# Kernel tuning notes

Hardware: AMD Instinct MI355X
Metric: run time of the kernel (lower is better)

The kernel has to match this reference:

```python
import jax, jax.numpy as jnp
import numpy as np

MAX_WAVELENGTH = 10000
BIG_NEG = -2.3819763e38

def _rope(x, positions):
    # x: [B, L, H, D], positions: [B, L] float32
    d = x.shape[-1]
    freq_exp = 2.0 / d * jnp.arange(d // 2, dtype=jnp.float32)
    timescale = MAX_WAVELENGTH ** freq_exp
    radians = (positions[..., None] / timescale[None, None, :])[..., None, :]  # [B,L,1,D/2]
    sin, cos = jnp.sin(radians), jnp.cos(radians)
    x1, x2 = jnp.split(x, 2, axis=-1)
    return jnp.concatenate([x1 * cos - x2 * sin, x2 * cos + x1 * sin], axis=-1).astype(x.dtype)

def _adaln_rmsnorm(x, cond, Wmod, bmod):
    # RMSNorm in fp32, then AdaLN scale/shift; returns (normed, gate[B,1,D])
    var = jnp.mean(jnp.square(x.astype(jnp.float32)), axis=-1, keepdims=True)
    normed = x * jax.lax.rsqrt(var + 1e-6)
    mod = (cond @ Wmod + bmod)[:, None, :]  # [B,1,3D]
    scale, shift, gate = jnp.split(mod, 3, axis=-1)
    return (normed * (1 + scale) + shift).astype(x.dtype), gate

def setup_inputs() -> dict:
    key = jax.random.key(0)
    ks = jax.random.split(key, 9)
    B, T, D, F, N, K, H = 2, 2048, 2048, 16384, 8, 1, 256
    x = jax.random.normal(ks[0], (B, T, D), jnp.float32)
    positions = jnp.broadcast_to(jnp.arange(T, dtype=jnp.float32), (B, T))
    attn_mask = jnp.broadcast_to(jnp.tril(jnp.ones((T, T), dtype=bool))[None, None], (B, 1, T, T))
    cond = jax.random.normal(ks[1], (B, D), jnp.float32)
    Wmod_a = jax.random.normal(ks[2], (D, 3 * D), jnp.float32) * 0.02
    bmod_a = jnp.zeros((3 * D,), jnp.float32)
    Wq = jax.random.normal(ks[3], (N, D, H), jnp.float32) * (D ** -0.5)
    Wkv = jax.random.normal(ks[4], (2, K, D, H), jnp.float32) * (D ** -0.5)
    Wo = jax.random.normal(ks[5], (N, H, D), jnp.float32) * ((N * H) ** -0.5)
    Wmod_f = jax.random.normal(ks[6], (D, 3 * D), jnp.float32) * 0.02
    bmod_f = jnp.zeros((3 * D,), jnp.float32)
    Wg = jax.random.normal(ks[7], (2, D, F), jnp.float32) * (D ** -0.5)
    Wl = jax.random.normal(ks[8], (F, D), jnp.float32) * (F ** -0.5)
    return dict(x=x, positions=positions, attn_mask=attn_mask, cond=cond,
                Wmod_a=Wmod_a, bmod_a=bmod_a, Wq=Wq, Wkv=Wkv, Wo=Wo,
                Wmod_f=Wmod_f, bmod_f=bmod_f, Wg=Wg, Wl=Wl)

def reference(x, positions, attn_mask, cond, Wmod_a, bmod_a, Wq, Wkv, Wo, Wmod_f, bmod_f, Wg, Wl):
    K = Wkv.shape[1]               # num_kv_heads
    H = Wq.shape[-1]               # head_dim
    # --- pre-attention AdaLN RMSNorm ---
    n, gate_a = _adaln_rmsnorm(x, cond, Wmod_a, bmod_a)
    # --- GQA projections ---
    q = jnp.einsum('BTD,NDH->BTNH', n, Wq)
    k = jnp.einsum('BSD,KDH->BSKH', n, Wkv[0])
    v = jnp.einsum('BSD,KDH->BSKH', n, Wkv[1])
    q = _rope(q, positions) * (H ** -0.5)
    k = _rope(k, positions)
    B, T, N, _ = q.shape
    q = q.reshape(B, T, K, N // K, H)  # B T K G H
    logits = jnp.einsum('BTKGH,BSKH->BKGTS', q, k, preferred_element_type=jnp.float32)
    masked = jnp.where(attn_mask[:, :, None, :, :], logits, BIG_NEG)
    probs = jax.nn.softmax(masked, axis=-1).astype(x.dtype)
    enc = jnp.einsum('BKGTS,BSKH->BTKGH', probs, v).reshape(B, T, N, H)
    attn_out = jnp.einsum('BTNH,NHD->BTD', enc, Wo)
    # gated residual
    x = x + attn_out * gate_a
    # --- pre-FFN AdaLN RMSNorm + gated-GeLU MLP ---
    n, gate_f = _adaln_rmsnorm(x, cond, Wmod_f, bmod_f)
    h = jax.nn.gelu(jnp.einsum('BTD,DF->BTF', n, Wg[0])) * jnp.einsum('BTD,DF->BTF', n, Wg[1])
    mlp_out = jnp.einsum('BTF,FD->BTD', h, Wl)
    return x + mlp_out * gate_f
```

## Files before the change

kernel.cpp:

```cpp
#include <hip/hip_runtime.h>
#include <hip/hip_bf16.h>

typedef __bf16 bf16_t;
typedef __bf16 bf16x8 __attribute__((ext_vector_type(8)));
typedef float  f32x4  __attribute__((ext_vector_type(4)));

#define DEV static __device__ __forceinline__

DEV void gload16(const bf16_t* g, bf16_t* l) {
    __builtin_amdgcn_global_load_lds(
        (const __attribute__((address_space(1))) void*)g,
        (__attribute__((address_space(3))) void*)l, 16, 0, 0);
}

enum { EPI_F32 = 0, EPI_BF16 = 1, EPI_RES = 2, EPI_GELU = 3, EPI_MUL = 4 };

template<int EPI>
__global__ __launch_bounds__(512, 1)
void gemm256(const bf16_t* __restrict__ A, const bf16_t* __restrict__ Bt,
             void* __restrict__ Cout, int Kd, int lda, int ldb, int ldc,
             long sCz,
             const float* __restrict__ res, const float* __restrict__ gate,
             int gateStride, int rowsPerB, const bf16_t* __restrict__ aux)
{
    const int nbx = gridDim.x;
    const int nwg = nbx * gridDim.y;
    int lin = blockIdx.y * nbx + blockIdx.x;
    const int q8 = nwg >> 3, r8 = nwg & 7;
    const int xcd = lin & 7, oo = lin >> 3;
    lin = (xcd < r8 ? xcd * (q8 + 1) : r8 * (q8 + 1) + (xcd - r8) * q8) + oo;
    const long m0 = (long)(lin / nbx) * 256;
    const long n0 = (long)(lin % nbx) * 256;
    const long kbase = (long)blockIdx.z * Kd;

    const int tid = threadIdx.x;
    const int l   = tid & 63;
    const int w   = tid >> 6;
    const int wr  = w >> 2;
    const int wcn = w & 3;

    __shared__ bf16_t sA[2][256 * 64];
    __shared__ bf16_t sB[2][256 * 64];

    const int  srow = w * 8 + (l >> 3);
    const long sgc  = (long)(((l & 7) ^ (l >> 3)) << 3);

    const int NT = Kd >> 6;

    auto STAGE = [&](const bf16_t* __restrict__ G, long row0, int ld, long kt, bf16_t* lb) {
#pragma unroll
        for (int L = 0; L < 4; L++) {
            const long g = (row0 + L * 64 + srow) * (long)ld + kt + sgc;
            gload16(G + g, lb + L * 4096 + w * 512);
        }
    };

    f32x4 acc[8][4];
#pragma unroll
    for (int i = 0; i < 8; i++)
#pragma unroll
        for (int j = 0; j < 4; j++) acc[i][j] = f32x4{0.f, 0.f, 0.f, 0.f};

    STAGE(A,  m0, lda, kbase, &sA[0][0]);
    STAGE(Bt, n0, ldb, kbase, &sB[0][0]);
    __syncthreads();

    const int co0 = ((l >> 4) ^ (l & 7)) << 3;
    const int co1 = ((4 + (l >> 4)) ^ (l & 7)) << 3;

    for (int t = 0; t < NT; ++t) {
        const int cur = t & 1;
        if (t + 1 < NT) {
            STAGE(A,  m0, lda, kbase + (long)(t + 1) * 64, &sA[cur ^ 1][0]);
            STAGE(Bt, n0, ldb, kbase + (long)(t + 1) * 64, &sB[cur ^ 1][0]);
        }
        const bf16_t* sAc = sA[cur];
        const bf16_t* sBc = sB[cur];
        bf16x8 a0[8], a1[8], b0[4], b1[4];
#pragma unroll
        for (int mi = 0; mi < 8; mi++) {
            const int row = wr * 128 + mi * 16 + (l & 15);
            a0[mi] = *(const bf16x8*)(&sAc[row * 64 + co0]);
            a1[mi] = *(const bf16x8*)(&sAc[row * 64 + co1]);
        }
#pragma unroll
        for (int nj = 0; nj < 4; nj++) {
            const int row = wcn * 64 + nj * 16 + (l & 15);
            b0[nj] = *(const bf16x8*)(&sBc[row * 64 + co0]);
            b1[nj] = *(const bf16x8*)(&sBc[row * 64 + co1]);
        }
#pragma unroll
        for (int mi = 0; mi < 8; mi++)
#pragma unroll
            for (int nj = 0; nj < 4; nj++)
                acc[mi][nj] = __builtin_amdgcn_mfma_f32_16x16x32_bf16(a0[mi], b0[nj], acc[mi][nj], 0, 0, 0);
#pragma unroll
        for (int mi = 0; mi < 8; mi++)
#pragma unroll
            for (int nj = 0; nj < 4; nj++)
                acc[mi][nj] = __builtin_amdgcn_mfma_f32_16x16x32_bf16(a1[mi], b1[nj], acc[mi][nj], 0, 0, 0);
        __syncthreads();
    }

#pragma unroll
    for (int mi = 0; mi < 8; mi++) {
#pragma unroll
        for (int nj = 0; nj < 4; nj++) {
            f32x4 v = acc[mi][nj];
            const long col   = n0 + wcn * 64 + nj * 16 + (l & 15);
            const long row0r = m0 + wr * 128 + mi * 16 + ((l >> 4) * 4);
#pragma unroll
            for (int e = 0; e < 4; e++) {
                const long row = row0r + e;
                const long idx = row * (long)ldc + col + (long)blockIdx.z * sCz;
                const float val = v[e];
                if constexpr (EPI == EPI_F32) {
                    ((float*)Cout)[idx] = val;
                } else if constexpr (EPI == EPI_BF16) {
                    ((bf16_t*)Cout)[idx] = (bf16_t)val;
                } else if constexpr (EPI == EPI_RES) {
                    const int b = (int)(row / rowsPerB);
                    ((float*)Cout)[idx] = res[row * (long)ldc + col] + val * gate[(long)b * gateStride + col];
                } else if constexpr (EPI == EPI_GELU) {
                    const float gl = 0.5f * val * (1.f + tanhf(0.7978845608f * (val + 0.044715f * val * val * val)));
                    ((bf16_t*)Cout)[idx] = (bf16_t)gl;
                } else if constexpr (EPI == EPI_MUL) {
                    ((bf16_t*)Cout)[idx] = (bf16_t)((float)aux[idx] * val);
                }
            }
        }
    }
}

__global__ __launch_bounds__(256)
void combine_splitk(const float* __restrict__ P, const float* __restrict__ X1,
                    const float* __restrict__ gate, float* __restrict__ out,
                    int D, int T, int gateStride, long zstride, long n4)
{
    for (long i4 = (long)blockIdx.x * 256 + threadIdx.x; i4 < n4; i4 += (long)gridDim.x * 256) {
        const long i = i4 * 4;
        const float4 p0 = *(const float4*)(P + i);
        const float4 p1 = *(const float4*)(P + i + zstride);
        const float4 xv = *(const float4*)(X1 + i);
        const long row = i / D;
        const int  b   = (int)(row / T);
        const int  col = (int)(i - row * D);
        const float* gp = gate + (long)b * gateStride + col;
        float4 r;
        r.x = xv.x + (p0.x + p1.x) * gp[0];
        r.y = xv.y + (p0.y + p1.y) * gp[1];
        r.z = xv.z + (p0.z + p1.z) * gp[2];
        r.w = xv.w + (p0.w + p1.w) * gp[3];
        *(float4*)(out + i) = r;
    }
}

template<int EPI, int CAUSAL>
__global__ __launch_bounds__(256)
void gemm_bt(const bf16_t* __restrict__ A, const bf16_t* __restrict__ Bt,
             void* __restrict__ Cout,
             int M, int N, int Kd, int lda, int ldb, int ldc,
             long sAz, long sBz, long sCz,
             const float* __restrict__ res, const float* __restrict__ gate,
             int gateStride, int rowsPerB, const bf16_t* __restrict__ aux)
{
    const int tid = threadIdx.x;
    const int l   = tid & 63;
    const int w   = tid >> 6;
    const int wr  = w >> 1, wc = w & 1;
    const long m0 = (long)blockIdx.y * 128;
    const long n0 = (long)blockIdx.x * 128;
    const int  z  = blockIdx.z;

    if constexpr (CAUSAL == 1) {
        if (n0 > m0 + 127) return;
    }
    int kend = Kd;
    if constexpr (CAUSAL == 2) {
        const int kc = (int)m0 + 128;
        kend = kc < Kd ? kc : Kd;
    }

    A  += (long)z * sAz;
    Bt += (long)z * sBz;

    __shared__ bf16_t As[128 * 32];
// ... 111 lines not shown
void rmsnorm_adaln(const float* __restrict__ xin, const float* __restrict__ mod,
                   bf16_t* __restrict__ out, int D, int T, int D3)
{
    const long row = blockIdx.x;
    const int  b   = (int)(row / T);
    const int  tid = threadIdx.x;
    const float4* x4 = (const float4*)(xin + row * (long)D);
    const float4 v0 = x4[tid], v1 = x4[tid + 256];
    float ss = v0.x * v0.x + v0.y * v0.y + v0.z * v0.z + v0.w * v0.w
             + v1.x * v1.x + v1.y * v1.y + v1.z * v1.z + v1.w * v1.w;
    for (int o = 32; o; o >>= 1) ss += __shfl_down(ss, o, 64);
    __shared__ float red[4];
    if ((tid & 63) == 0) red[tid >> 6] = ss;
    __syncthreads();
    ss = red[0] + red[1] + red[2] + red[3];
    const float rs = rsqrtf(ss / (float)D + 1e-6f);
    const float* sc = mod + (long)b * D3;
    const float* sh = sc + D;
    const float4 s0 = ((const float4*)sc)[tid], s1 = ((const float4*)sc)[tid + 256];
    const float4 h0 = ((const float4*)sh)[tid], h1 = ((const float4*)sh)[tid + 256];
    bf16_t* orow = out + row * (long)D;
    orow[tid * 4 + 0]         = (bf16_t)(v0.x * rs * (1.f + s0.x) + h0.x);
    orow[tid * 4 + 1]         = (bf16_t)(v0.y * rs * (1.f + s0.y) + h0.y);
    orow[tid * 4 + 2]         = (bf16_t)(v0.z * rs * (1.f + s0.z) + h0.z);
    orow[tid * 4 + 3]         = (bf16_t)(v0.w * rs * (1.f + s0.w) + h0.w);
    orow[(tid + 256) * 4 + 0] = (bf16_t)(v1.x * rs * (1.f + s1.x) + h1.x);
    orow[(tid + 256) * 4 + 1] = (bf16_t)(v1.y * rs * (1.f + s1.y) + h1.y);
    orow[(tid + 256) * 4 + 2] = (bf16_t)(v1.z * rs * (1.f + s1.z) + h1.z);
    orow[(tid + 256) * 4 + 3] = (bf16_t)(v1.w * rs * (1.f + s1.w) + h1.w);
}

__global__ __launch_bounds__(128)
void rope_q(const bf16_t* __restrict__ qp, const float* __restrict__ positions,
            bf16_t* __restrict__ qo, int T, int NH, int H)
{
    const int t = blockIdx.x, n = blockIdx.y, b = blockIdx.z;
    const int i = threadIdx.x;
    const long in0 = ((long)(b * T + t)) * NH + n * H;
    const float x1 = (float)qp[in0 + i];
    const float x2 = (float)qp[in0 + i + 128];
    const float pos = positions[b * T + t];
    const float inv = expf(-9.210340371976184f * (float)i / 128.f);
    float s, c;
    sincosf(pos * inv, &s, &c);
    const float scl = 0.0625f;
    const long out0 = (((long)(b * 8 + n)) * T + t) * H;
    qo[out0 + i]       = (bf16_t)((x1 * c - x2 * s) * scl);
    qo[out0 + i + 128] = (bf16_t)((x2 * c + x1 * s) * scl);
}

__global__ __launch_bounds__(128)
void rope_kv(const bf16_t* __restrict__ kvp, const float* __restrict__ positions,
             bf16_t* __restrict__ ko, bf16_t* __restrict__ vt, int T, int H, int S)
{
    const int t = blockIdx.x, b = blockIdx.y;
    const int i = threadIdx.x;
    const long in0 = ((long)(b * T + t)) * 512;
    const float k1 = (float)kvp[in0 + i];
    const float k2 = (float)kvp[in0 + i + 128];
    const float pos = positions[b * T + t];
    const float inv = expf(-9.210340371976184f * (float)i / 128.f);
    float s, c;
    sincosf(pos * inv, &s, &c);
    const long ko0 = ((long)(b * T + t)) * H;
    ko[ko0 + i]       = (bf16_t)(k1 * c - k2 * s);
    ko[ko0 + i + 128] = (bf16_t)(k2 * c + k1 * s);
    vt[((long)b * H + i) * S + t]       = kvp[in0 + 256 + i];
    vt[((long)b * H + i + 128) * S + t] = kvp[in0 + 256 + i + 128];
}

__global__ __launch_bounds__(256)
void softmax_causal(const float* __restrict__ sc, bf16_t* __restrict__ pr, int T, int S)
{
    const int t = blockIdx.x, g = blockIdx.y;
    const long row = (long)g * T + t;
    const float* srow = sc + row * S;
    bf16_t* prow = pr + row * S;
    const int tid = threadIdx.x;
    const int limit = t | 127;
    const int nch = (limit >> 8) + 1;
    float vals[8];
    float mx = -3.4e38f;
    for (int i = 0; i < nch; i++) {
        const int s = i * 256 + tid;
        const float v = (s <= t) ? srow[s] : -3.4e38f;
        vals[i] = v;
        mx = fmaxf(mx, v);
    }
    for (int o = 32; o; o >>= 1) mx = fmaxf(mx, __shfl_down(mx, o, 64));
    __shared__ float red[4];
// ... 7 lines not shown
        const float e = (s <= t) ? __expf(vals[i] - mx) : 0.f;
        vals[i] = e;
        sum += e;
    }
    for (int o = 32; o; o >>= 1) sum += __shfl_down(sum, o, 64);
    if ((tid & 63) == 0) red[tid >> 6] = sum;
    __syncthreads();
    sum = red[0] + red[1] + red[2] + red[3];
    const float invs = 1.f / sum;
    for (int i = 0; i < nch; i++)
        prow[i * 256 + tid] = (bf16_t)(vals[i] * invs);
}

extern "C" void kernel_launch(void* const* d_in, const int* in_sizes, int n_in,
                              void* d_out, int out_size, void* d_ws, size_t ws_size,
                              hipStream_t stream)
{
    const float* x      = (const float*)d_in[0];
    const float* pos    = (const float*)d_in[1];
    const float* cond   = (const float*)d_in[3];
    const float* Wmod_a = (const float*)d_in[4];
    const float* bmod_a = (const float*)d_in[5];
    const float* Wq     = (const float*)d_in[6];
    const float* Wkv    = (const float*)d_in[7];
    const float* Wo     = (const float*)d_in[8];
    const float* Wmod_f = (const float*)d_in[9];
    const float* bmod_f = (const float*)d_in[10];
    const float* Wg     = (const float*)d_in[11];
    const float* Wl     = (const float*)d_in[12];

    constexpr int  Bb = 2, T = 2048, D = 2048, F = 16384, Nh = 8, H = 256;
    constexpr int  NH = 2048, S = 2048, G = 8, BT = 4096, D3 = 6144;
    constexpr int  KSLICE = 64, NZ = D / KSLICE;

    char* ws = (char*)d_ws;
    size_t off = 0;
    auto alloc = [&](size_t bytes) { char* p = ws + off; off += bytes; return p; };

    bf16_t* WQT  = (bf16_t*)alloc((size_t)NH * D * 2);
    bf16_t* WKVT = (bf16_t*)alloc((size_t)512 * D * 2);
    bf16_t* WOT  = (bf16_t*)alloc((size_t)D * NH * 2);
    bf16_t* WGT  = (bf16_t*)alloc((size_t)2 * F * D * 2);
    bf16_t* WLT  = (bf16_t*)alloc((size_t)D * F * 2);
    float*  MODA = (float*)alloc((size_t)Bb * D3 * 4);
    float*  MODF = (float*)alloc((size_t)Bb * D3 * 4);
    float*  PART = (float*)alloc((size_t)NZ * Bb * D3 * 4);
    bf16_t* NA   = (bf16_t*)alloc((size_t)BT * D * 2);
    bf16_t* QP   = (bf16_t*)alloc((size_t)BT * NH * 2);
    bf16_t* KVP  = (bf16_t*)alloc((size_t)BT * 512 * 2);
    bf16_t* Qr   = (bf16_t*)alloc((size_t)Bb * Nh * T * H * 2);
    bf16_t* Kr   = (bf16_t*)alloc((size_t)Bb * T * H * 2);
    bf16_t* VT   = (bf16_t*)alloc((size_t)Bb * H * S * 2);
    bf16_t* ENC  = (bf16_t*)alloc((size_t)BT * NH * 2);
    float*  X1   = (float*)alloc((size_t)BT * D * 4);
    bf16_t* NF   = (bf16_t*)alloc((size_t)BT * D * 2);
    const size_t scBytes = (size_t)G * T * S * 4;
    const size_t prBytes = (size_t)G * T * S * 2;
    const size_t hBytes  = (size_t)BT * F * 2;
    const size_t bigBytes = (scBytes + prBytes > hBytes) ? (scBytes + prBytes) : hBytes;
    char* big = alloc(bigBytes);
    float*  SC = (float*)big;
    bf16_t* PR = (bf16_t*)(big + scBytes);
    bf16_t* Hb = (bf16_t*)big;
    float*  PARTK = (float*)(big + hBytes);
    (void)ws_size; (void)in_sizes; (void)n_in; (void)out_size;

    const dim3 tb(32, 8);
    transpose_f2b<<<dim3(H / 32, D / 32, 8), tb, 0, stream>>>(Wq,  WQT,  D,  H, (long)D * H, (long)H * D);
    transpose_f2b<<<dim3(H / 32, D / 32, 2), tb, 0, stream>>>(Wkv, WKVT, D,  H, (long)D * H, (long)H * D);
    transpose_f2b<<<dim3(D / 32, NH / 32, 1), tb, 0, stream>>>(Wo, WOT, NH,  D, 0, 0);
    transpose_f2b<<<dim3(F / 32, D / 32, 2), tb, 0, stream>>>(Wg,  WGT,  D,  F, (long)D * F, (long)F * D);
    transpose_f2b<<<dim3(D / 32, F / 32, 1), tb, 0, stream>>>(Wl,  WLT,  F,  D, 0, 0);
    modk_part<<<dim3(D3 / 256, Bb, NZ), 256, 0, stream>>>(cond, Wmod_a, PART, D3, KSLICE);
    modk_reduce<<<dim3(D3 / 256, Bb), 256, 0, stream>>>(PART, bmod_a, MODA, D3, NZ);
    modk_part<<<dim3(D3 / 256, Bb, NZ), 256, 0, stream>>>(cond, Wmod_f, PART, D3, KSLICE);
    modk_reduce<<<dim3(D3 / 256, Bb), 256, 0, stream>>>(PART, bmod_f, MODF, D3, NZ);
    rmsnorm_adaln<<<BT, 256, 0, stream>>>(x, MODA, NA, D, T, D3);
    gemm256<EPI_BF16><<<dim3(NH / 256, BT / 256, 1), 512, 0, stream>>>(
        NA, WQT, QP, D, D, D, NH, 0, nullptr, nullptr, 0, 0, nullptr);
    gemm_bt<EPI_BF16, 0><<<dim3(512 / 128, BT / 128, 1), 256, 0, stream>>>(
        NA, WKVT, KVP, BT, 512, D, D, D, 512, 0, 0, 0, nullptr, nullptr, 0, 0, nullptr);
    rope_q<<<dim3(T, Nh, Bb), 128, 0, stream>>>(QP, pos, Qr, T, NH, H);
    rope_kv<<<dim3(T, Bb), 128, 0, stream>>>(KVP, pos, Kr, VT, T, H, S);
    for (int b = 0; b < Bb; b++) {
        gemm_bt<EPI_F32, 1><<<dim3(S / 128, T / 128, G), 256, 0, stream>>>(
            Qr + (long)b * Nh * T * H, Kr + (long)b * T * H, SC,
            T, S, H, H, H, S, (long)T * H, 0, (long)T * S, nullptr, nullptr, 0, 0, nullptr);
        softmax_causal<<<dim3(T, G), 256, 0, stream>>>(SC, PR, T, S);
        gemm_bt<EPI_BF16, 2><<<dim3(H / 128, T / 128, G), 256, 0, stream>>>(
            PR, VT + (long)b * H * S, ENC + (long)b * T * NH,
            T, H, S, S, S, NH, (long)T * S, 0, (long)H, nullptr, nullptr, 0, 0, nullptr);
    }
    gemm256<EPI_RES><<<dim3(D / 256, BT / 256, 1), 512, 0, stream>>>(
        ENC, WOT, X1, NH, NH, NH, D, 0, x, MODA + 2 * D, D3, T, nullptr);
    rmsnorm_adaln<<<BT, 256, 0, stream>>>(X1, MODF, NF, D, T, D3);
    gemm256<EPI_GELU><<<dim3(F / 256, BT / 256, 1), 512, 0, stream>>>(
        NF, WGT, Hb, D, D, D, F, 0, nullptr, nullptr, 0, 0, nullptr);
    gemm256<EPI_MUL><<<dim3(F / 256, BT / 256, 1), 512, 0, stream>>>(
        NF, WGT + (long)F * D, Hb, D, D, D, F, 0, nullptr, nullptr, 0, 0, Hb);
    gemm256<EPI_F32><<<dim3(D / 256, BT / 256, 2), 512, 0, stream>>>(
        Hb, WLT, PARTK, F / 2, F, F, D, (long)BT * D, nullptr, nullptr, 0, 0, nullptr);
    combine_splitk<<<2048, 256, 0, stream>>>(
        PARTK, X1, MODF + 2 * D, (float*)d_out, D, T, D3, (long)BT * D, (long)BT * D / 4);
}
```

Measured before the change: 1.689 ms.

## Replace 256x256 GEMM with triple-buffered 256x128 tile kernel, drop split-K

Replaces the double-buffered 256x256 GEMM with a 256x128-tile kernel that uses three LDS buffers. It prefetches two K-tiles ahead, uses explicit vmcnt waits with raw barriers, and raises wave priority around the MFMA block. The final down-projection no longer uses split-K plus a combine kernel; it runs as a single-pass GEMM with a fused residual-gate epilogue. The smaller tiles give more workgroups and deeper prefetch, but they increase global traffic per FLOP, and the down-projection now has a long serial K loop.

```diff
diff --git a/kernel.cpp b/kernel.cpp
--- a/kernel.cpp
+++ b/kernel.cpp
@@ -17,9 +17,8 @@
 
 template<int EPI>
 __global__ __launch_bounds__(512, 1)
-void gemm256(const bf16_t* __restrict__ A, const bf16_t* __restrict__ Bt,
+void gemm_p3(const bf16_t* __restrict__ A, const bf16_t* __restrict__ Bt,
              void* __restrict__ Cout, int Kd, int lda, int ldb, int ldc,
-             long sCz,
              const float* __restrict__ res, const float* __restrict__ gate,
              int gateStride, int rowsPerB, const bf16_t* __restrict__ aux)
 {
@@ -30,56 +29,55 @@
     const int xcd = lin & 7, oo = lin >> 3;
     lin = (xcd < r8 ? xcd * (q8 + 1) : r8 * (q8 + 1) + (xcd - r8) * q8) + oo;
     const long m0 = (long)(lin / nbx) * 256;
-    const long n0 = (long)(lin % nbx) * 256;
-    const long kbase = (long)blockIdx.z * Kd;
+    const long n0 = (long)(lin % nbx) * 128;
 
     const int tid = threadIdx.x;
     const int l   = tid & 63;
     const int w   = tid >> 6;
-    const int wr  = w >> 2;
-    const int wcn = w & 3;
-
-    __shared__ bf16_t sA[2][256 * 64];
-    __shared__ bf16_t sB[2][256 * 64];
-
-    const int  srow = w * 8 + (l >> 3);
-    const long sgc  = (long)(((l & 7) ^ (l >> 3)) << 3);
-
+    const int wrm = w >> 1;
+    const int wcn = w & 1;
+
+    __shared__ bf16_t sA[3][16384];
+    __shared__ bf16_t sB[3][8192];
+
+    const long sgc = (long)(((l & 7) ^ (l >> 3)) << 3);
     const int NT = Kd >> 6;
 
-    auto STAGE = [&](const bf16_t* __restrict__ G, long row0, int ld, long kt, bf16_t* lb) {
-#pragma unroll
-        for (int L = 0; L < 4; L++) {
-            const long g = (row0 + L * 64 + srow) * (long)ld + kt + sgc;
-            gload16(G + g, lb + L * 4096 + w * 512);
-        }
+    auto STAGE = [&](long kt, int bi) {
+#pragma unroll
+        for (int L = 0; L < 4; L++)
+            gload16(A + (m0 + L * 64 + w * 8 + (l >> 3)) * (long)lda + kt + sgc,
+                    &sA[bi][L * 4096 + w * 512]);
+#pragma unroll
+        for (int L = 0; L < 2; L++)
+            gload16(Bt + (n0 + L * 64 + w * 8 + (l >> 3)) * (long)ldb + kt + sgc,
+                    &sB[bi][L * 4096 + w * 512]);
     };
 
-    f32x4 acc[8][4];
-#pragma unroll
-    for (int i = 0; i < 8; i++)
+    f32x4 acc[4][4];
+#pragma unroll
+    for (int i = 0; i < 4; i++)
 #pragma unroll
         for (int j = 0; j < 4; j++) acc[i][j] = f32x4{0.f, 0.f, 0.f, 0.f};
-
-    STAGE(A,  m0, lda, kbase, &sA[0][0]);
-    STAGE(Bt, n0, ldb, kbase, &sB[0][0]);
-    __syncthreads();
 
     const int co0 = ((l >> 4) ^ (l & 7)) << 3;
     const int co1 = ((4 + (l >> 4)) ^ (l & 7)) << 3;
 
+    STAGE(0, 0);
+    STAGE(64, 1);
+    asm volatile("s_waitcnt vmcnt(6)" ::: "memory");
+    __builtin_amdgcn_s_barrier();
+
     for (int t = 0; t < NT; ++t) {
-        const int cur = t & 1;
-        if (t + 1 < NT) {
-            STAGE(A,  m0, lda, kbase + (long)(t + 1) * 64, &sA[cur ^ 1][0]);
-            STAGE(Bt, n0, ldb, kbase + (long)(t + 1) * 64, &sB[cur ^ 1][0]);
-        }
-        const bf16_t* sAc = sA[cur];
-        const bf16_t* sBc = sB[cur];
-        bf16x8 a0[8], a1[8], b0[4], b1[4];
-#pragma unroll
-        for (int mi = 0; mi < 8; mi++) {
-            const int row = wr * 128 + mi * 16 + (l & 15);
+        const int bi = t % 3;
+        if (t + 2 < NT) STAGE((long)(t + 2) * 64, (t + 2) % 3);
+
+        const bf16_t* sAc = sA[bi];
+        const bf16_t* sBc = sB[bi];
+        bf16x8 a0[4], a1[4], b0[4], b1[4];
+#pragma unroll
+        for (int mi = 0; mi < 4; mi++) {
+            const int row = wrm * 64 + mi * 16 + (l & 15);
             a0[mi] = *(const bf16x8*)(&sAc[row * 64 + co0]);
             a1[mi] = *(const bf16x8*)(&sAc[row * 64 + co1]);
         }
@@ -89,30 +87,38 @@
             b0[nj] = *(const bf16x8*)(&sBc[row * 64 + co0]);
             b1[nj] = *(const bf16x8*)(&sBc[row * 64 + co1]);
         }
-#pragma unroll
-        for (int mi = 0; mi < 8; mi++)
+        __builtin_amdgcn_s_setprio(1);
+#pragma unroll
+        for (int mi = 0; mi < 4; mi++)
 #pragma unroll
             for (int nj = 0; nj < 4; nj++)
                 acc[mi][nj] = __builtin_amdgcn_mfma_f32_16x16x32_bf16(a0[mi], b0[nj], acc[mi][nj], 0, 0, 0);
 #pragma unroll
-        for (int mi = 0; mi < 8; mi++)
+        for (int mi = 0; mi < 4; mi++)
 #pragma unroll
             for (int nj = 0; nj < 4; nj++)
                 acc[mi][nj] = __builtin_amdgcn_mfma_f32_16x16x32_bf16(a1[mi], b1[nj], acc[mi][nj], 0, 0, 0);
-        __syncthreads();
-    }
-
-#pragma unroll
-    for (int mi = 0; mi < 8; mi++) {
+        __builtin_amdgcn_s_setprio(0);
+
+        if (t + 2 < NT) {
+            asm volatile("s_waitcnt vmcnt(6)" ::: "memory");
+        } else if (t + 1 < NT) {
+            asm volatile("s_waitcnt vmcnt(0)" ::: "memory");
+        }
+        __builtin_amdgcn_s_barrier();
+    }
+
+#pragma unroll
+    for (int mi = 0; mi < 4; mi++) {
 #pragma unroll
         for (int nj = 0; nj < 4; nj++) {
             f32x4 v = acc[mi][nj];
             const long col   = n0 + wcn * 64 + nj * 16 + (l & 15);
-            const long row0r = m0 + wr * 128 + mi * 16 + ((l >> 4) * 4);
+            const long row0r = m0 + wrm * 64 + mi * 16 + ((l >> 4) * 4);
 #pragma unroll
             for (int e = 0; e < 4; e++) {
                 const long row = row0r + e;
-                const long idx = row * (long)ldc + col + (long)blockIdx.z * sCz;
+                const long idx = row * (long)ldc + col;
                 const float val = v[e];
                 if constexpr (EPI == EPI_F32) {
                     ((float*)Cout)[idx] = val;
@@ -129,29 +135,6 @@
                 }
             }
         }
-    }
-}
-
-__global__ __launch_bounds__(256)
-void combine_splitk(const float* __restrict__ P, const float* __restrict__ X1,
-                    const float* __restrict__ gate, float* __restrict__ out,
-                    int D, int T, int gateStride, long zstride, long n4)
-{
-    for (long i4 = (long)blockIdx.x * 256 + threadIdx.x; i4 < n4; i4 += (long)gridDim.x * 256) {
-        const long i = i4 * 4;
-        const float4 p0 = *(const float4*)(P + i);
-        const float4 p1 = *(const float4*)(P + i + zstride);
-        const float4 xv = *(const float4*)(X1 + i);
-        const long row = i / D;
-        const int  b   = (int)(row / T);
-        const int  col = (int)(i - row * D);
-        const float* gp = gate + (long)b * gateStride + col;
-        float4 r;
-        r.x = xv.x + (p0.x + p1.x) * gp[0];
-        r.y = xv.y + (p0.y + p1.y) * gp[1];
-        r.z = xv.z + (p0.z + p1.z) * gp[2];
-        r.w = xv.w + (p0.w + p1.w) * gp[3];
-        *(float4*)(out + i) = r;
     }
 }
 
@@ -456,7 +439,6 @@
     float*  SC = (float*)big;
     bf16_t* PR = (bf16_t*)(big + scBytes);
     bf16_t* Hb = (bf16_t*)big;
-    float*  PARTK = (float*)(big + hBytes);
     (void)ws_size; (void)in_sizes; (void)n_in; (void)out_size;
 
     const dim3 tb(32, 8);
@@ -470,8 +452,8 @@
     modk_part<<<dim3(D3 / 256, Bb, NZ), 256, 0, stream>>>(cond, Wmod_f, PART, D3, KSLICE);
     modk_reduce<<<dim3(D3 / 256, Bb), 256, 0, stream>>>(PART, bmod_f, MODF, D3, NZ);
     rmsnorm_adaln<<<BT, 256, 0, stream>>>(x, MODA, NA, D, T, D3);
-    gemm256<EPI_BF16><<<dim3(NH / 256, BT / 256, 1), 512, 0, stream>>>(
-        NA, WQT, QP, D, D, D, NH, 0, nullptr, nullptr, 0, 0, nullptr);
+    gemm_p3<EPI_BF16><<<dim3(NH / 128, BT / 256), 512, 0, stream>>>(
+        NA, WQT, QP, D, D, D, NH, nullptr, nullptr, 0, 0, nullptr);
     gemm_bt<EPI_BF16, 0><<<dim3(512 / 128, BT / 128, 1), 256, 0, stream>>>(
         NA, WKVT, KVP, BT, 512, D, D, D, 512, 0, 0, 0, nullptr, nullptr, 0, 0, nullptr);
     rope_q<<<dim3(T, Nh, Bb), 128, 0, stream>>>(QP, pos, Qr, T, NH, H);
@@ -485,15 +467,13 @@
             PR, VT + (long)b * H * S, ENC + (long)b * T * NH,
             T, H, S, S, S, NH, (long)T * S, 0, (long)H, nullptr, nullptr, 0, 0, nullptr);
     }
-    gemm256<EPI_RES><<<dim3(D / 256, BT / 256, 1), 512, 0, stream>>>(
-        ENC, WOT, X1, NH, NH, NH, D, 0, x, MODA + 2 * D, D3, T, nullptr);
+    gemm_p3<EPI_RES><<<dim3(D / 128, BT / 256), 512, 0, stream>>>(
+        ENC, WOT, X1, NH, NH, NH, D, x, MODA + 2 * D, D3, T, nullptr);
     rmsnorm_adaln<<<BT, 256, 0, stream>>>(X1, MODF, NF, D, T, D3);
-    gemm256<EPI_GELU><<<dim3(F / 256, BT / 256, 1), 512, 0, stream>>>(
-        NF, WGT, Hb, D, D, D, F, 0, nullptr, nullptr, 0, 0, nullptr);
-    gemm256<EPI_MUL><<<dim3(F / 256, BT / 256, 1), 512, 0, stream>>>(
-        NF, WGT + (long)F * D, Hb, D, D, D, F, 0, nullptr, nullptr, 0, 0, Hb);
-    gemm256<EPI_F32><<<dim3(D / 256, BT / 256, 2), 512, 0, stream>>>(
-        Hb, WLT, PARTK, F / 2, F, F, D, (long)BT * D, nullptr, nullptr, 0, 0, nullptr);
-    combine_splitk<<<2048, 256, 0, stream>>>(
-        PARTK, X1, MODF + 2 * D, (float*)d_out, D, T, D3, (long)BT * D, (long)BT * D / 4);
-}
+    gemm_p3<EPI_GELU><<<dim3(F / 128, BT / 256), 512, 0, stream>>>(
+        NF, WGT, Hb, D, D, D, F, nullptr, nullptr, 0, 0, nullptr);
+    gemm_p3<EPI_MUL><<<dim3(F / 128, BT / 256), 512, 0, stream>>>(
+        NF, WGT + (long)F * D, Hb, D, D, D, F, nullptr, nullptr, 0, 0, Hb);
+    gemm_p3<EPI_RES><<<dim3(D / 128, BT / 256), 512, 0, stream>>>(
+        Hb, WLT, (float*)d_out, F, F, F, D, X1, MODF + 2 * D, D3, T, nullptr);
+}
```

Measured after the change: 1.956 ms. 15.8% more time.

## Rewrite 256x256 GEMM as 8-phase interleaved pipeline and fuse QKV projection

Applied to the files above, without the earlier changes.

Replaces the double-buffered GEMM main loop with an 8-phase schedule. Each phase loads a quarter of the A/B fragments from LDS, issues a few global->LDS chunk loads for upcoming K tiles, and runs 16 MFMAs under raised wave priority. Explicit vmcnt waits and barriers replace the per-tile __syncthreads. The goal is to overlap global loads, LDS reads and MFMA issue more finely. The Q and KV projections are also merged into one 2560-wide GEMM, which relies on the K/V weights sitting right after the Q weights in the workspace, and the rope kernels now take a row stride.

```diff
diff --git a/kernel.cpp b/kernel.cpp
--- a/kernel.cpp
+++ b/kernel.cpp
@@ -15,13 +15,43 @@
 
 enum { EPI_F32 = 0, EPI_BF16 = 1, EPI_RES = 2, EPI_GELU = 3, EPI_MUL = 4 };
 
+#define MFMA16(QQ, AR, BR)                                                    \
+  _Pragma("unroll")                                                           \
+  for (int nj = 0; nj < 4; nj++) {                                            \
+    acc[(QQ)*4+0][nj] = __builtin_amdgcn_mfma_f32_16x16x32_bf16(AR[0], BR[nj], acc[(QQ)*4+0][nj], 0, 0, 0); \
+    acc[(QQ)*4+1][nj] = __builtin_amdgcn_mfma_f32_16x16x32_bf16(AR[1], BR[nj], acc[(QQ)*4+1][nj], 0, 0, 0); \
+    acc[(QQ)*4+2][nj] = __builtin_amdgcn_mfma_f32_16x16x32_bf16(AR[2], BR[nj], acc[(QQ)*4+2][nj], 0, 0, 0); \
+    acc[(QQ)*4+3][nj] = __builtin_amdgcn_mfma_f32_16x16x32_bf16(AR[3], BR[nj], acc[(QQ)*4+3][nj], 0, 0, 0); \
+  }
+
+#define READA(SAc, QQ, CO, AR)                                                \
+  _Pragma("unroll")                                                           \
+  for (int mi = 0; mi < 4; mi++)                                              \
+    AR[mi] = *(const bf16x8*)(&SAc[(wr*128 + (QQ)*64 + mi*16 + (l & 15))*64 + (CO)]);
+
+#define READB(SBc, CO, BR)                                                    \
+  _Pragma("unroll")                                                           \
+  for (int nj = 0; nj < 4; nj++)                                              \
+    BR[nj] = *(const bf16x8*)(&SBc[(wcn*64 + nj*16 + (l & 15))*64 + (CO)]);
+
+#define PHASE(RD_STMT, QQ, AR, BR, STAGE_STMT, WAIT_STMT)                     \
+  { RD_STMT STAGE_STMT                                                        \
+    __builtin_amdgcn_s_barrier();                                             \
+    asm volatile("s_waitcnt lgkmcnt(0)" ::: "memory");                        \
+    __builtin_amdgcn_sched_barrier(0);                                        \
+    __builtin_amdgcn_s_setprio(1);                                            \
+    MFMA16(QQ, AR, BR);                                                       \
+    __builtin_amdgcn_s_setprio(0);                                            \
+    WAIT_STMT                                                                 \
+    __builtin_amdgcn_s_barrier(); }
+
 template<int EPI>
 __global__ __launch_bounds__(512, 1)
-void gemm256(const bf16_t* __restrict__ A, const bf16_t* __restrict__ Bt,
-             void* __restrict__ Cout, int Kd, int lda, int ldb, int ldc,
-             long sCz,
-             const float* __restrict__ res, const float* __restrict__ gate,
-             int gateStride, int rowsPerB, const bf16_t* __restrict__ aux)
+void gemm8p(const bf16_t* __restrict__ A, const bf16_t* __restrict__ Bt,
+            void* __restrict__ Cout, int Kd, int lda, int ldb, int ldc,
+            long sCz,
+            const float* __restrict__ res, const float* __restrict__ gate,
+            int gateStride, int rowsPerB, const bf16_t* __restrict__ aux)
 {
     const int nbx = gridDim.x;
     const int nwg = nbx * gridDim.y;
@@ -31,7 +61,7 @@
     lin = (xcd < r8 ? xcd * (q8 + 1) : r8 * (q8 + 1) + (xcd - r8) * q8) + oo;
     const long m0 = (long)(lin / nbx) * 256;
     const long n0 = (long)(lin % nbx) * 256;
-    const long kbase = (long)blockIdx.z * Kd;
+    const long kb = (long)blockIdx.z * Kd;
 
     const int tid = threadIdx.x;
     const int l   = tid & 63;
@@ -39,67 +69,67 @@
     const int wr  = w >> 2;
     const int wcn = w & 3;
 
-    __shared__ bf16_t sA[2][256 * 64];
-    __shared__ bf16_t sB[2][256 * 64];
-
-    const int  srow = w * 8 + (l >> 3);
-    const long sgc  = (long)(((l & 7) ^ (l >> 3)) << 3);
-
+    __shared__ bf16_t sA[2][16384];
+    __shared__ bf16_t sB[2][16384];
+
+    const long sgc = (long)(((l & 7) ^ (l >> 3)) << 3);
     const int NT = Kd >> 6;
-
-    auto STAGE = [&](const bf16_t* __restrict__ G, long row0, int ld, long kt, bf16_t* lb) {
-#pragma unroll
-        for (int L = 0; L < 4; L++) {
-            const long g = (row0 + L * 64 + srow) * (long)ld + kt + sgc;
-            gload16(G + g, lb + L * 4096 + w * 512);
-        }
+    const int NI = NT >> 1;
+
+    auto SCA = [&](long kt, int bi, int c) {
+        gload16(A + (m0 + c * 64 + w * 8 + (l >> 3)) * (long)lda + kt + sgc,
+                &sA[bi][c * 4096 + w * 512]);
     };
+    auto SCB = [&](long kt, int bi, int c) {
+        gload16(Bt + (n0 + c * 64 + w * 8 + (l >> 3)) * (long)ldb + kt + sgc,
+                &sB[bi][c * 4096 + w * 512]);
+    };
 
     f32x4 acc[8][4];
 #pragma unroll
     for (int i = 0; i < 8; i++)
 #pragma unroll
         for (int j = 0; j < 4; j++) acc[i][j] = f32x4{0.f, 0.f, 0.f, 0.f};
-
-    STAGE(A,  m0, lda, kbase, &sA[0][0]);
-    STAGE(Bt, n0, ldb, kbase, &sB[0][0]);
-    __syncthreads();
 
     const int co0 = ((l >> 4) ^ (l & 7)) << 3;
     const int co1 = ((4 + (l >> 4)) ^ (l & 7)) << 3;
 
-    for (int t = 0; t < NT; ++t) {
-        const int cur = t & 1;
-        if (t + 1 < NT) {
-            STAGE(A,  m0, lda, kbase + (long)(t + 1) * 64, &sA[cur ^ 1][0]);
-            STAGE(Bt, n0, ldb, kbase + (long)(t + 1) * 64, &sB[cur ^ 1][0]);
-        }
-        const bf16_t* sAc = sA[cur];
-        const bf16_t* sBc = sB[cur];
-        bf16x8 a0[8], a1[8], b0[4], b1[4];
-#pragma unroll
-        for (int mi = 0; mi < 8; mi++) {
-            const int row = wr * 128 + mi * 16 + (l & 15);
-            a0[mi] = *(const bf16x8*)(&sAc[row * 64 + co0]);
-            a1[mi] = *(const bf16x8*)(&sAc[row * 64 + co1]);
-        }
-#pragma unroll
-        for (int nj = 0; nj < 4; nj++) {
-            const int row = wcn * 64 + nj * 16 + (l & 15);
-            b0[nj] = *(const bf16x8*)(&sBc[row * 64 + co0]);
-            b1[nj] = *(const bf16x8*)(&sBc[row * 64 + co1]);
-        }
-#pragma unroll
-        for (int mi = 0; mi < 8; mi++)
-#pragma unroll
-            for (int nj = 0; nj < 4; nj++)
-                acc[mi][nj] = __builtin_amdgcn_mfma_f32_16x16x32_bf16(a0[mi], b0[nj], acc[mi][nj], 0, 0, 0);
-#pragma unroll
-        for (int mi = 0; mi < 8; mi++)
-#pragma unroll
-            for (int nj = 0; nj < 4; nj++)
-                acc[mi][nj] = __builtin_amdgcn_mfma_f32_16x16x32_bf16(a1[mi], b1[nj], acc[mi][nj], 0, 0, 0);
-        __syncthreads();
+    SCA(kb, 0, 0); SCA(kb, 0, 1); SCA(kb, 0, 2); SCA(kb, 0, 3);
+    SCB(kb, 0, 0); SCB(kb, 0, 1); SCB(kb, 0, 2); SCB(kb, 0, 3);
+    SCA(kb + 64, 1, 0); SCA(kb + 64, 1, 2); SCB(kb + 64, 1, 0); SCB(kb + 64, 1, 1);
+    asm volatile("s_waitcnt vmcnt(4)" ::: "memory");
+    __builtin_amdgcn_s_barrier();
+
+    bf16x8 b0[4], b1[4], aR[4];
+    const bf16_t* sA0p = sA[0]; const bf16_t* sB0p = sB[0];
+    const bf16_t* sA1p = sA[1]; const bf16_t* sB1p = sB[1];
+
+    for (int it = 0; it < NI; ++it) {
+        const long kv  = kb + (long)(2 * it + 1) * 64;
+        const long kc  = kb + (long)(2 * it + 2) * 64;
+        const long kd2 = kb + (long)(2 * it + 3) * 64;
+        const bool hc  = (2 * it + 2) < NT;
+
+        PHASE({ READB(sB0p, co0, b0); READA(sA0p, 0, co0, aR); }, 0, aR, b0,
+              { SCB(kv, 1, 2); SCB(kv, 1, 3); }, {})
+        PHASE({ READB(sB0p, co1, b1); READA(sA0p, 0, co1, aR); }, 0, aR, b1,
+              { SCA(kv, 1, 1); SCA(kv, 1, 3); }, {})
+        PHASE({ READA(sA0p, 1, co0, aR); }, 1, aR, b0,
+              { if (hc) { SCA(kc, 0, 0); SCA(kc, 0, 2); } }, {})
+        PHASE({ READA(sA0p, 1, co1, aR); }, 1, aR, b1,
+              { if (hc) { SCB(kc, 0, 0); SCB(kc, 0, 1); } },
+              { if (hc) { asm volatile("s_waitcnt vmcnt(4)" ::: "memory"); }
+                else    { asm volatile("s_waitcnt vmcnt(0)" ::: "memory"); } })
+        PHASE({ READB(sB1p, co0, b0); READA(sA1p, 0, co0, aR); }, 0, aR, b0,
+              { if (hc) { SCB(kc, 0, 2); SCB(kc, 0, 3); } }, {})
+        PHASE({ READB(sB1p, co1, b1); READA(sA1p, 0, co1, aR); }, 0, aR, b1,
+              { if (hc) { SCA(kc, 0, 1); SCA(kc, 0, 3); } }, {})
+        PHASE({ READA(sA1p, 1, co0, aR); }, 1, aR, b0,
+              { if (hc) { SCA(kd2, 1, 0); SCA(kd2, 1, 2); } }, {})
+        PHASE({ READA(sA1p, 1, co1, aR); }, 1, aR, b1,
+              { if (hc) { SCB(kd2, 1, 0); SCB(kd2, 1, 1); } },
+              { if (hc) { asm volatile("s_waitcnt vmcnt(4)" ::: "memory"); }
+                else    { asm volatile("s_waitcnt vmcnt(0)" ::: "memory"); } })
     }
 
 #pragma unroll
@@ -108,7 +138,7 @@
         for (int nj = 0; nj < 4; nj++) {
             f32x4 v = acc[mi][nj];
             const long col   = n0 + wcn * 64 + nj * 16 + (l & 15);
-            const long row0r = m0 + wr * 128 + mi * 16 + ((l >> 4) * 4);
+            const long row0r = m0 + (mi >> 2) * 0 + wr * 128 + mi * 16 + ((l >> 4) * 4);
 #pragma unroll
             for (int e = 0; e < 4; e++) {
                 const long row = row0r + e;
@@ -329,11 +359,11 @@
 
 __global__ __launch_bounds__(128)
 void rope_q(const bf16_t* __restrict__ qp, const float* __restrict__ positions,
-            bf16_t* __restrict__ qo, int T, int NH, int H)
+            bf16_t* __restrict__ qo, int T, int ldq, int H)
 {
     const int t = blockIdx.x, n = blockIdx.y, b = blockIdx.z;
     const int i = threadIdx.x;
-    const long in0 = ((long)(b * T + t)) * NH + n * H;
+    const long in0 = ((long)(b * T + t)) * ldq + n * H;
     const float x1 = (float)qp[in0 + i];
     const float x2 = (float)qp[in0 + i + 128];
     const float pos = positions[b * T + t];
@@ -348,11 +378,11 @@
 
 __global__ __launch_bounds__(128)
 void rope_kv(const bf16_t* __restrict__ kvp, const float* __restrict__ positions,
-             bf16_t* __restrict__ ko, bf16_t* __restrict__ vt, int T, int H, int S)
+             bf16_t* __restrict__ ko, bf16_t* __restrict__ vt, int T, int H, int S, int ldkv)
 {
     const int t = blockIdx.x, b = blockIdx.y;
     const int i = threadIdx.x;
-    const long in0 = ((long)(b * T + t)) * 512;
+    const long in0 = ((long)(b * T + t)) * ldkv;
     const float k1 = (float)kvp[in0 + i];
     const float k2 = (float)kvp[in0 + i + 128];
     const float pos = positions[b * T + t];
@@ -426,6 +456,7 @@
     constexpr int  Bb = 2, T = 2048, D = 2048, F = 16384, Nh = 8, H = 256;
     constexpr int  NH = 2048, S = 2048, G = 8, BT = 4096, D3 = 6144;
     constexpr int  KSLICE = 64, NZ = D / KSLICE;
+    constexpr int  NQKV = 2560;
 
     char* ws = (char*)d_ws;
     size_t off = 0;
@@ -440,8 +471,7 @@
     float*  MODF = (float*)alloc((size_t)Bb * D3 * 4);
     float*  PART = (float*)alloc((size_t)NZ * Bb * D3 * 4);
     bf16_t* NA   = (bf16_t*)alloc((size_t)BT * D * 2);
-    bf16_t* QP   = (bf16_t*)alloc((size_t)BT * NH * 2);
-    bf16_t* KVP  = (bf16_t*)alloc((size_t)BT * 512 * 2);
+    bf16_t* QKVP = (bf16_t*)alloc((size_t)BT * NQKV * 2);
     bf16_t* Qr   = (bf16_t*)alloc((size_t)Bb * Nh * T * H * 2);
     bf16_t* Kr   = (bf16_t*)alloc((size_t)Bb * T * H * 2);
     bf16_t* VT   = (bf16_t*)alloc((size_t)Bb * H * S * 2);
@@ -470,12 +500,10 @@
     modk_part<<<dim3(D3 / 256, Bb, NZ), 256, 0, stream>>>(cond, Wmod_f, PART, D3, KSLICE);
     modk_reduce<<<dim3(D3 / 256, Bb), 256, 0, stream>>>(PART, bmod_f, MODF, D3, NZ);
     rmsnorm_adaln<<<BT, 256, 0, stream>>>(x, MODA, NA, D, T, D3);
-    gemm256<EPI_BF16><<<dim3(NH / 256, BT / 256, 1), 512, 0, stream>>>(
-        NA, WQT, QP, D, D, D, NH, 0, nullptr, nullptr, 0, 0, nullptr);
-    gemm_bt<EPI_BF16, 0><<<dim3(512 / 128, BT / 128, 1), 256, 0, stream>>>(
-        NA, WKVT, KVP, BT, 512, D, D, D, 512, 0, 0, 0, nullptr, nullptr, 0, 0, nullptr);
-    rope_q<<<dim3(T, Nh, Bb), 128, 0, stream>>>(QP, pos, Qr, T, NH, H);
-    rope_kv<<<dim3(T, Bb), 128, 0, stream>>>(KVP, pos, Kr, VT, T, H, S);
+    gemm8p<EPI_BF16><<<dim3(NQKV / 256, BT / 256, 1), 512, 0, stream>>>(
+        NA, WQT, QKVP, D, D, D, NQKV, 0, nullptr, nullptr, 0, 0, nullptr);
+    rope_q<<<dim3(T, Nh, Bb), 128, 0, stream>>>(QKVP, pos, Qr, T, NQKV, H);
+    rope_kv<<<dim3(T, Bb), 128, 0, stream>>>(QKVP + NH, pos, Kr, VT, T, H, S, NQKV);
     for (int b = 0; b < Bb; b++) {
         gemm_bt<EPI_F32, 1><<<dim3(S / 128, T / 128, G), 256, 0, stream>>>(
             Qr + (long)b * Nh * T * H, Kr + (long)b * T * H, SC,
@@ -485,14 +513,14 @@
             PR, VT + (long)b * H * S, ENC + (long)b * T * NH,
             T, H, S, S, S, NH, (long)T * S, 0, (long)H, nullptr, nullptr, 0, 0, nullptr);
     }
-    gemm256<EPI_RES><<<dim3(D / 256, BT / 256, 1), 512, 0, stream>>>(
+    gemm8p<EPI_RES><<<dim3(D / 256, BT / 256, 1), 512, 0, stream>>>(
         ENC, WOT, X1, NH, NH, NH, D, 0, x, MODA + 2 * D, D3, T, nullptr);
     rmsnorm_adaln<<<BT, 256, 0, stream>>>(X1, MODF, NF, D, T, D3);
-    gemm256<EPI_GELU><<<dim3(F / 256, BT / 256, 1), 512, 0, stream>>>(
+    gemm8p<EPI_GELU><<<dim3(F / 256, BT / 256, 1), 512, 0, stream>>>(
         NF, WGT, Hb, D, D, D, F, 0, nullptr, nullptr, 0, 0, nullptr);
-    gemm256<EPI_MUL><<<dim3(F / 256, BT / 256, 1), 512, 0, stream>>>(
+    gemm8p<EPI_MUL><<<dim3(F / 256, BT / 256, 1), 512, 0, stream>>>(
         NF, WGT + (long)F * D, Hb, D, D, D, F, 0, nullptr, nullptr, 0, 0, Hb);
-    gemm256<EPI_F32><<<dim3(D / 256, BT / 256, 2), 512, 0, stream>>>(
+    gemm8p<EPI_F32><<<dim3(D / 256, BT / 256, 2), 512, 0, stream>>>(
         Hb, WLT, PARTK, F / 2, F, F, D, (long)BT * D, nullptr, nullptr, 0, 0, nullptr);
     combine_splitk<<<2048, 256, 0, stream>>>(
         PARTK, X1, MODF + 2 * D, (float*)d_out, D, T, D3, (long)BT * D, (long)BT * D / 4);
```

After: 1.609 ms. 4.8% less time.

## Switch GEMMs to 128x256 tiles with 32x32 MFMA and fuse QKV projection

Applied to the files above, without the earlier changes.

The main GEMM kernel moves from 256x256 tiles with a 64-wide K step and 16x16x32 MFMA to 128x256 tiles with a 32-wide K step and 32x32x16 MFMA. It raises the launch-bounds occupancy hint, shrinks shared memory per block, and raises wave priority around the MFMA block. The Q and KV projections are fused into one GEMM writing a combined 2560-wide buffer, which assumes the KV weights sit right after the Q weights in the workspace; the rope kernels now take a row stride. The aim is more concurrent blocks and fewer launches, at the cost of less data reuse per tile and more barriers per K step.

```diff
diff --git a/kernel.cpp b/kernel.cpp
--- a/kernel.cpp
+++ b/kernel.cpp
@@ -4,6 +4,7 @@
 typedef __bf16 bf16_t;
 typedef __bf16 bf16x8 __attribute__((ext_vector_type(8)));
 typedef float  f32x4  __attribute__((ext_vector_type(4)));
+typedef float  f32x16 __attribute__((ext_vector_type(16)));
 
 #define DEV static __device__ __forceinline__
 
@@ -16,12 +17,12 @@
 enum { EPI_F32 = 0, EPI_BF16 = 1, EPI_RES = 2, EPI_GELU = 3, EPI_MUL = 4 };
 
 template<int EPI>
-__global__ __launch_bounds__(512, 1)
-void gemm256(const bf16_t* __restrict__ A, const bf16_t* __restrict__ Bt,
-             void* __restrict__ Cout, int Kd, int lda, int ldb, int ldc,
-             long sCz,
-             const float* __restrict__ res, const float* __restrict__ gate,
-             int gateStride, int rowsPerB, const bf16_t* __restrict__ aux)
+__global__ __launch_bounds__(512, 4)
+void gemm32(const bf16_t* __restrict__ A, const bf16_t* __restrict__ Bt,
+            void* __restrict__ Cout, int Kd, int lda, int ldb, int ldc,
+            long sCz,
+            const float* __restrict__ res, const float* __restrict__ gate,
+            int gateStride, int rowsPerB, const bf16_t* __restrict__ aux)
 {
     const int nbx = gridDim.x;
     const int nwg = nbx * gridDim.y;
@@ -29,91 +30,89 @@
     const int q8 = nwg >> 3, r8 = nwg & 7;
     const int xcd = lin & 7, oo = lin >> 3;
     lin = (xcd < r8 ? xcd * (q8 + 1) : r8 * (q8 + 1) + (xcd - r8) * q8) + oo;
-    const long m0 = (long)(lin / nbx) * 256;
+    const long m0 = (long)(lin / nbx) * 128;
     const long n0 = (long)(lin % nbx) * 256;
-    const long kbase = (long)blockIdx.z * Kd;
+    const long kb = (long)blockIdx.z * Kd;
 
     const int tid = threadIdx.x;
     const int l   = tid & 63;
     const int w   = tid >> 6;
-    const int wr  = w >> 2;
+    const int wrm = w >> 2;
     const int wcn = w & 3;
 
-    __shared__ bf16_t sA[2][256 * 64];
-    __shared__ bf16_t sB[2][256 * 64];
-
-    const int  srow = w * 8 + (l >> 3);
-    const long sgc  = (long)(((l & 7) ^ (l >> 3)) << 3);
-
-    const int NT = Kd >> 6;
-
-    auto STAGE = [&](const bf16_t* __restrict__ G, long row0, int ld, long kt, bf16_t* lb) {
-#pragma unroll
-        for (int L = 0; L < 4; L++) {
-            const long g = (row0 + L * 64 + srow) * (long)ld + kt + sgc;
-            gload16(G + g, lb + L * 4096 + w * 512);
-        }
+    __shared__ bf16_t sA[2][128 * 32];
+    __shared__ bf16_t sB[2][256 * 32];
+
+    const long sgc = (long)(((l & 3) ^ ((l >> 3) & 3)) << 3);
+    const int NT = Kd >> 5;
+
+    auto STAGE = [&](long kt, int bi) {
+        gload16(A + (m0 + w * 16 + (l >> 2)) * (long)lda + kt + sgc,
+                &sA[bi][w * 512]);
+#pragma unroll
+        for (int L = 0; L < 2; L++)
+            gload16(Bt + (n0 + L * 128 + w * 16 + (l >> 2)) * (long)ldb + kt + sgc,
+                    &sB[bi][L * 4096 + w * 512]);
     };
 
-    f32x4 acc[8][4];
-#pragma unroll
-    for (int i = 0; i < 8; i++)
-#pragma unroll
-        for (int j = 0; j < 4; j++) acc[i][j] = f32x4{0.f, 0.f, 0.f, 0.f};
-
-    STAGE(A,  m0, lda, kbase, &sA[0][0]);
-    STAGE(Bt, n0, ldb, kbase, &sB[0][0]);
-    __syncthreads();
-
-    const int co0 = ((l >> 4) ^ (l & 7)) << 3;
-    const int co1 = ((4 + (l >> 4)) ^ (l & 7)) << 3;
+    f32x16 acc[2][2];
+#pragma unroll
+    for (int i = 0; i < 2; i++)
+#pragma unroll
+        for (int j = 0; j < 2; j++)
+#pragma unroll
+            for (int e = 0; e < 16; e++) acc[i][j][e] = 0.f;
+
+    const int co0 = (((0 + (l >> 5)) ^ ((l >> 1) & 3)) << 3);
+    const int co1 = (((2 + (l >> 5)) ^ ((l >> 1) & 3)) << 3);
+
+    STAGE(kb, 0);
+    __syncthreads();
 
     for (int t = 0; t < NT; ++t) {
         const int cur = t & 1;
-        if (t + 1 < NT) {
-            STAGE(A,  m0, lda, kbase + (long)(t + 1) * 64, &sA[cur ^ 1][0]);
-            STAGE(Bt, n0, ldb, kbase + (long)(t + 1) * 64, &sB[cur ^ 1][0]);
-        }
+        if (t + 1 < NT) STAGE(kb + (long)(t + 1) * 32, cur ^ 1);
+
         const bf16_t* sAc = sA[cur];
         const bf16_t* sBc = sB[cur];
-        bf16x8 a0[8], a1[8], b0[4], b1[4];
-#pragma unroll
-        for (int mi = 0; mi < 8; mi++) {
-            const int row = wr * 128 + mi * 16 + (l & 15);
-            a0[mi] = *(const bf16x8*)(&sAc[row * 64 + co0]);
-            a1[mi] = *(const bf16x8*)(&sAc[row * 64 + co1]);
+        bf16x8 af[2][2], bfv[2][2];
+#pragma unroll
+        for (int mi = 0; mi < 2; mi++) {
+            const int r = (wrm * 64 + mi * 32 + (l & 31)) * 32;
+            af[mi][0] = *(const bf16x8*)(&sAc[r + co0]);
+            af[mi][1] = *(const bf16x8*)(&sAc[r + co1]);
         }
 #pragma unroll
-        for (int nj = 0; nj < 4; nj++) {
-            const int row = wcn * 64 + nj * 16 + (l & 15);
-            b0[nj] = *(const bf16x8*)(&sBc[row * 64 + co0]);
-            b1[nj] = *(const bf16x8*)(&sBc[row * 64 + co1]);
+        for (int nj = 0; nj < 2; nj++) {
+            const int r = (wcn * 64 + nj * 32 + (l & 31)) * 32;
+            bfv[nj][0] = *(const bf16x8*)(&sBc[r + co0]);
+            bfv[nj][1] = *(const bf16x8*)(&sBc[r + co1]);
         }
-#pragma unroll
-        for (int mi = 0; mi < 8; mi++)
-#pragma unroll
-            for (int nj = 0; nj < 4; nj++)
-                acc[mi][nj] = __builtin_amdgcn_mfma_f32_16x16x32_bf16(a0[mi], b0[nj], acc[mi][nj], 0, 0, 0);
-#pragma unroll
-        for (int mi = 0; mi < 8; mi++)
-#pragma unroll
-            for (int nj = 0; nj < 4; nj++)
-                acc[mi][nj] = __builtin_amdgcn_mfma_f32_16x16x32_bf16(a1[mi], b1[nj], acc[mi][nj], 0, 0, 0);
+        __builtin_amdgcn_s_setprio(1);
+#pragma unroll
+        for (int kc = 0; kc < 2; kc++)
+#pragma unroll
+            for (int mi = 0; mi < 2; mi++)
+#pragma unroll
+                for (int nj = 0; nj < 2; nj++)
+                    acc[mi][nj] = __builtin_amdgcn_mfma_f32_32x32x16_bf16(
+                        af[mi][kc], bfv[nj][kc], acc[mi][nj], 0, 0, 0);
+        __builtin_amdgcn_s_setprio(0);
         __syncthreads();
     }
 
 #pragma unroll
-    for (int mi = 0; mi < 8; mi++) {
-#pragma unroll
-        for (int nj = 0; nj < 4; nj++) {
-            f32x4 v = acc[mi][nj];
-            const long col   = n0 + wcn * 64 + nj * 16 + (l & 15);
-            const long row0r = m0 + wr * 128 + mi * 16 + ((l >> 4) * 4);
-#pragma unroll
-            for (int e = 0; e < 4; e++) {
-                const long row = row0r + e;
+    for (int mi = 0; mi < 2; mi++) {
+#pragma unroll
+        for (int nj = 0; nj < 2; nj++) {
+            const f32x16 v = acc[mi][nj];
+            const long col   = n0 + wcn * 64 + nj * 32 + (l & 31);
+            const long rbase = m0 + wrm * 64 + mi * 32 + 4 * (l >> 5);
+#pragma unroll
+            for (int reg = 0; reg < 16; reg++) {
+                const long row = rbase + (reg & 3) + 8 * (reg >> 2);
                 const long idx = row * (long)ldc + col + (long)blockIdx.z * sCz;
-                const float val = v[e];
+                const float val = v[reg];
                 if constexpr (EPI == EPI_F32) {
                     ((float*)Cout)[idx] = val;
                 } else if constexpr (EPI == EPI_BF16) {
@@ -329,11 +328,11 @@
 
 __global__ __launch_bounds__(128)
 void rope_q(const bf16_t* __restrict__ qp, const float* __restrict__ positions,
-            bf16_t* __restrict__ qo, int T, int NH, int H)
+            bf16_t* __restrict__ qo, int T, int ldq, int H)
 {
     const int t = blockIdx.x, n = blockIdx.y, b = blockIdx.z;
     const int i = threadIdx.x;
-    const long in0 = ((long)(b * T + t)) * NH + n * H;
+    const long in0 = ((long)(b * T + t)) * ldq + n * H;
     const float x1 = (float)qp[in0 + i];
     const float x2 = (float)qp[in0 + i + 128];
     const float pos = positions[b * T + t];
@@ -348,11 +347,11 @@
 
 __global__ __launch_bounds__(128)
 void rope_kv(const bf16_t* __restrict__ kvp, const float* __restrict__ positions,
-             bf16_t* __restrict__ ko, bf16_t* __restrict__ vt, int T, int H, int S)
+             bf16_t* __restrict__ ko, bf16_t* __restrict__ vt, int T, int H, int S, int ldkv)
 {
     const int t = blockIdx.x, b = blockIdx.y;
     const int i = threadIdx.x;
-    const long in0 = ((long)(b * T + t)) * 512;
+    const long in0 = ((long)(b * T + t)) * ldkv;
     const float k1 = (float)kvp[in0 + i];
     const float k2 = (float)kvp[in0 + i + 128];
     const float pos = positions[b * T + t];
@@ -426,6 +425,7 @@
     constexpr int  Bb = 2, T = 2048, D = 2048, F = 16384, Nh = 8, H = 256;
     constexpr int  NH = 2048, S = 2048, G = 8, BT = 4096, D3 = 6144;
     constexpr int  KSLICE = 64, NZ = D / KSLICE;
+    constexpr int  NQKV = 2560;
 
     char* ws = (char*)d_ws;
     size_t off = 0;
@@ -440,8 +440,7 @@
     float*  MODF = (float*)alloc((size_t)Bb * D3 * 4);
     float*  PART = (float*)alloc((size_t)NZ * Bb * D3 * 4);
     bf16_t* NA   = (bf16_t*)alloc((size_t)BT * D * 2);
-    bf16_t* QP   = (bf16_t*)alloc((size_t)BT * NH * 2);
-    bf16_t* KVP  = (bf16_t*)alloc((size_t)BT * 512 * 2);
+    bf16_t* QKVP = (bf16_t*)alloc((size_t)BT * NQKV * 2);
     bf16_t* Qr   = (bf16_t*)alloc((size_t)Bb * Nh * T * H * 2);
     bf16_t* Kr   = (bf16_t*)alloc((size_t)Bb * T * H * 2);
     bf16_t* VT   = (bf16_t*)alloc((size_t)Bb * H * S * 2);
@@ -470,12 +469,10 @@
     modk_part<<<dim3(D3 / 256, Bb, NZ), 256, 0, stream>>>(cond, Wmod_f, PART, D3, KSLICE);
     modk_reduce<<<dim3(D3 / 256, Bb), 256, 0, stream>>>(PART, bmod_f, MODF, D3, NZ);
     rmsnorm_adaln<<<BT, 256, 0, stream>>>(x, MODA, NA, D, T, D3);
-    gemm256<EPI_BF16><<<dim3(NH / 256, BT / 256, 1), 512, 0, stream>>>(
-        NA, WQT, QP, D, D, D, NH, 0, nullptr, nullptr, 0, 0, nullptr);
-    gemm_bt<EPI_BF16, 0><<<dim3(512 / 128, BT / 128, 1), 256, 0, stream>>>(
-        NA, WKVT, KVP, BT, 512, D, D, D, 512, 0, 0, 0, nullptr, nullptr, 0, 0, nullptr);
-    rope_q<<<dim3(T, Nh, Bb), 128, 0, stream>>>(QP, pos, Qr, T, NH, H);
-    rope_kv<<<dim3(T, Bb), 128, 0, stream>>>(KVP, pos, Kr, VT, T, H, S);
+    gemm32<EPI_BF16><<<dim3(NQKV / 256, BT / 128, 1), 512, 0, stream>>>(
+        NA, WQT, QKVP, D, D, D, NQKV, 0, nullptr, nullptr, 0, 0, nullptr);
+    rope_q<<<dim3(T, Nh, Bb), 128, 0, stream>>>(QKVP, pos, Qr, T, NQKV, H);
+    rope_kv<<<dim3(T, Bb), 128, 0, stream>>>(QKVP + NH, pos, Kr, VT, T, H, S, NQKV);
     for (int b = 0; b < Bb; b++) {
         gemm_bt<EPI_F32, 1><<<dim3(S / 128, T / 128, G), 256, 0, stream>>>(
             Qr + (long)b * Nh * T * H, Kr + (long)b * T * H, SC,
@@ -485,14 +482,14 @@
             PR, VT + (long)b * H * S, ENC + (long)b * T * NH,
             T, H, S, S, S, NH, (long)T * S, 0, (long)H, nullptr, nullptr, 0, 0, nullptr);
     }
-    gemm256<EPI_RES><<<dim3(D / 256, BT / 256, 1), 512, 0, stream>>>(
+    gemm32<EPI_RES><<<dim3(D / 256, BT / 128, 1), 512, 0, stream>>>(
         ENC, WOT, X1, NH, NH, NH, D, 0, x, MODA + 2 * D, D3, T, nullptr);
     rmsnorm_adaln<<<BT, 256, 0, stream>>>(X1, MODF, NF, D, T, D3);
-    gemm256<EPI_GELU><<<dim3(F / 256, BT / 256, 1), 512, 0, stream>>>(
+    gemm32<EPI_GELU><<<dim3(F / 256, BT / 128, 1), 512, 0, stream>>>(
         NF, WGT, Hb, D, D, D, F, 0, nullptr, nullptr, 0, 0, nullptr);
-    gemm256<EPI_MUL><<<dim3(F / 256, BT / 256, 1), 512, 0, stream>>>(
+    gemm32<EPI_MUL><<<dim3(F / 256, BT / 128, 1), 512, 0, stream>>>(
         NF, WGT + (long)F * D, Hb, D, D, D, F, 0, nullptr, nullptr, 0, 0, Hb);
-    gemm256<EPI_F32><<<dim3(D / 256, BT / 256, 2), 512, 0, stream>>>(
+    gemm32<EPI_F32><<<dim3(D / 256, BT / 128, 2), 512, 0, stream>>>(
         Hb, WLT, PARTK, F / 2, F, F, D, (long)BT * D, nullptr, nullptr, 0, 0, nullptr);
     combine_splitk<<<2048, 256, 0, stream>>>(
         PARTK, X1, MODF + 2 * D, (float*)d_out, D, T, D3, (long)BT * D, (long)BT * D / 4);
```

Result: slower. 1.765 ms (+4.4%).
